# Kernel optimization log

Measured on AMD Instinct MI355X. Metric: run time of the kernel, lower is better.

Reference implementation:

```python
import jax, jax.numpy as jnp
import numpy as np

NUM_CP = 5
DEGREE = 4
GRID_LO, GRID_HI = -1.0, 1.0
G = 3  # grid points, set via set_grid_points(3)


def _precompute_basis():
    # knots = linspace(lo - degree*0.1, hi + degree*0.1, num_cp + degree + 1)
    knots = np.linspace(GRID_LO - DEGREE * 0.1, GRID_HI + DEGREE * 0.1, NUM_CP + DEGREE + 1)
    grid_points = np.linspace(GRID_LO, GRID_HI, G)
    basis = np.zeros((G, NUM_CP), dtype=np.float32)
    for i in range(NUM_CP):
        center = (knots[i + DEGREE // 2] + knots[i + DEGREE // 2 + 1]) / 2.0
        width = (knots[i + DEGREE + 1] - knots[i]) / 2.0
        basis[:, i] = np.exp(-((grid_points - center) / width) ** 2)
    basis_sum = basis.sum(axis=1, keepdims=True)
    return (basis / (basis_sum + 1e-6)).astype(np.float32)


def setup_inputs() -> dict:
    key = jax.random.key(0)
    k1, k2, k3, k4 = jax.random.split(key, 4)
    x = jax.random.normal(k1, (8, 2048, 2048), dtype=jnp.float32)
    control_points = jax.random.normal(k2, (NUM_CP,), dtype=jnp.float32) * 0.1
    base_weight = jax.random.normal(k3, (1,), dtype=jnp.float32)
    spline_weight = jax.random.normal(k4, (1,), dtype=jnp.float32)
    basis_values = jnp.asarray(_precompute_basis())
    return {"x": x, "control_points": control_points, "base_weight": base_weight,
            "spline_weight": spline_weight, "basis_values": basis_values}


def reference(x, control_points, base_weight, spline_weight, basis_values):
    x_clipped = jnp.clip(x, GRID_LO, GRID_HI)
    norm_x = (x_clipped - GRID_LO) / (GRID_HI - GRID_LO)
    grid_idx = norm_x * (G - 1)
    idx_low = jnp.clip(jnp.floor(grid_idx).astype(jnp.int32), 0, G - 1)
    idx_high = jnp.clip(jnp.ceil(grid_idx).astype(jnp.int32), 0, G - 1)
    frac = grid_idx - idx_low.astype(grid_idx.dtype)
    basis_low = basis_values[idx_low]    # [..., NUM_CP]
    basis_high = basis_values[idx_high]  # [..., NUM_CP]
    basis = basis_low * (1.0 - frac[..., None]) + basis_high * frac[..., None]
    y_spline = jnp.einsum('...c,c->...', basis, control_points)
    base = x * jax.nn.sigmoid(x)  # SiLU base_func
    return base_weight * base + spline_weight * y_spline
```

## Files before the change

### kernel.cpp

```cpp
#include <hip/hip_runtime.h>
#include <math.h>


typedef float f32x4 __attribute__((ext_vector_type(4)));

#define TPB 256
#define VPT 4

__device__ __forceinline__ float fast_rcp(float a) {
#if defined(__has_builtin)
#if __has_builtin(__builtin_amdgcn_rcpf)
    return __builtin_amdgcn_rcpf(a);
#else
    return 1.0f / a;
#endif
#else
    return 1.0f / a;
#endif
}

__global__ __launch_bounds__(TPB) void bspline_act_v5(
    const f32x4* __restrict__ x4,
    const float* __restrict__ cp,
    const float* __restrict__ bw_p,
    const float* __restrict__ sw_p,
    const float* __restrict__ bv,
    f32x4*       __restrict__ out4,
    int n4)
{
    const float c0 = cp[0], c1 = cp[1], c2 = cp[2], c3 = cp[3], c4 = cp[4];
    const float s0 = bv[0]*c0  + bv[1]*c1  + bv[2]*c2  + bv[3]*c3  + bv[4]*c4;
    const float s1 = bv[5]*c0  + bv[6]*c1  + bv[7]*c2  + bv[8]*c3  + bv[9]*c4;
    const float s2 = bv[10]*c0 + bv[11]*c1 + bv[12]*c2 + bv[13]*c3 + bv[14]*c4;
    const float bw = bw_p[0], sw = sw_p[0];
    const float S1 = sw * s1;
    const float D0 = sw * (s1 - s0);
    const float D1 = sw * (s2 - s1);

    const int base = blockIdx.x * (TPB * VPT) + threadIdx.x;

    f32x4 v[VPT];
#pragma unroll
    for (int k = 0; k < VPT; ++k) {
        const int idx = base + k * TPB;
        if (idx < n4) {
            v[k] = __builtin_nontemporal_load(&x4[idx]);
        } else {
            f32x4 z = {0.f, 0.f, 0.f, 0.f};
            v[k] = z;
        }
    }

#pragma unroll
    for (int k = 0; k < VPT; ++k) {
        const int idx = base + k * TPB;
        f32x4 xv = v[k];
        f32x4 r;
#pragma unroll
        for (int e = 0; e < 4; ++e) {
            float x  = xv[e];
            float u  = fminf(fmaxf(x, -1.0f), 1.0f);
            float ys = fmaf(D0, fminf(u, 0.0f),
                       fmaf(D1, fmaxf(u, 0.0f), S1));
            float ex  = __expf(-x);
            float sig = fast_rcp(1.0f + ex);
            r[e] = fmaf(bw * x, sig, ys);
        }
        if (idx < n4) __builtin_nontemporal_store(r, &out4[idx]);
    }
}

__global__ void bspline_act_tail(
    const float* __restrict__ x,
    const float* __restrict__ cp,
    const float* __restrict__ bw_p,
    const float* __restrict__ sw_p,
    const float* __restrict__ bv,
    float*       __restrict__ out,
    int start, int n)
{
    int i = start + blockIdx.x * blockDim.x + threadIdx.x;
    if (i >= n) return;
    const float c0 = cp[0], c1 = cp[1], c2 = cp[2], c3 = cp[3], c4 = cp[4];
    const float s0 = bv[0]*c0  + bv[1]*c1  + bv[2]*c2  + bv[3]*c3  + bv[4]*c4;
    const float s1 = bv[5]*c0  + bv[6]*c1  + bv[7]*c2  + bv[8]*c3  + bv[9]*c4;
    const float s2 = bv[10]*c0 + bv[11]*c1 + bv[12]*c2 + bv[13]*c3 + bv[14]*c4;
    const float bw = bw_p[0], sw = sw_p[0];
    const float S1 = sw * s1;
    const float D0 = sw * (s1 - s0);
    const float D1 = sw * (s2 - s1);

    float xv = x[i];
    float u  = fminf(fmaxf(xv, -1.0f), 1.0f);
    float ys = fmaf(D0, fminf(u, 0.0f), fmaf(D1, fmaxf(u, 0.0f), S1));
    float ex  = __expf(-xv);
    float sig = fast_rcp(1.0f + ex);
    out[i] = fmaf(bw * xv, sig, ys);
}

extern "C" void kernel_launch(void* const* d_in, const int* in_sizes, int n_in,
                              void* d_out, int out_size, void* d_ws, size_t ws_size,
                              hipStream_t stream) {
    const float* x  = (const float*)d_in[0];
    const float* cp = (const float*)d_in[1];
    const float* bw = (const float*)d_in[2];
    const float* sw = (const float*)d_in[3];
    const float* bv = (const float*)d_in[4];
    float* out = (float*)d_out;

    const int n  = in_sizes[0];
    const int n4 = n / 4;
    const int rem_start = n4 * 4;

    if (n4 > 0) {
        const int per_block = TPB * VPT;
        const int grid = (n4 + per_block - 1) / per_block;
        bspline_act_v5<<<grid, TPB, 0, stream>>>(
            (const f32x4*)x, cp, bw, sw, bv, (f32x4*)out, n4);
    }
    if (rem_start < n) {
        const int rem = n - rem_start;
        bspline_act_tail<<<(rem + 255) / 256, 256, 0, stream>>>(
            x, cp, bw, sw, bv, out, rem_start, n);
    }
}
```

Before: 226.0 us.

## Switch to grid-stride loop with capped grid and plain loads

Replaces the one-tile-per-block launch with a persistent grid-stride loop capped at a fixed number of blocks, each thread processing four strided vectors per iteration. Loads are now ordinary cached loads instead of nontemporal, and the sigmoid uses a full-precision division instead of the hardware reciprocal builtin. The aim is to cut block launch overhead and keep more loads in flight; the cost is that a fixed grid cap may underfill the device, and the exact division adds extra ALU work.

After: 244.6 us. +8.2%, slower.

```diff
diff --git a/kernel.cpp b/kernel.cpp
--- a/kernel.cpp
+++ b/kernel.cpp
@@ -4,22 +4,11 @@
 
 typedef float f32x4 __attribute__((ext_vector_type(4)));
 
-#define TPB 256
-#define VPT 4
+#define TPB    256
+#define UNROLL 4
+#define MAXBLK 2048
 
-__device__ __forceinline__ float fast_rcp(float a) {
-#if defined(__has_builtin)
-#if __has_builtin(__builtin_amdgcn_rcpf)
-    return __builtin_amdgcn_rcpf(a);
-#else
-    return 1.0f / a;
-#endif
-#else
-    return 1.0f / a;
-#endif
-}
-
-__global__ __launch_bounds__(TPB) void bspline_act_v5(
+__global__ __launch_bounds__(TPB) void bspline_act_v6(
     const f32x4* __restrict__ x4,
     const float* __restrict__ cp,
     const float* __restrict__ bw_p,
@@ -37,24 +26,33 @@
     const float D0 = sw * (s1 - s0);
     const float D1 = sw * (s2 - s1);
 
-    const int base = blockIdx.x * (TPB * VPT) + threadIdx.x;
+    const int stride = gridDim.x * TPB;
+    int i = blockIdx.x * TPB + threadIdx.x;
 
-    f32x4 v[VPT];
+    for (; i + 3 * stride < n4; i += UNROLL * stride) {
+        f32x4 v0 = x4[i];
+        f32x4 v1 = x4[i + stride];
+        f32x4 v2 = x4[i + 2 * stride];
+        f32x4 v3 = x4[i + 3 * stride];
+        f32x4 vin[UNROLL] = {v0, v1, v2, v3};
 #pragma unroll
-    for (int k = 0; k < VPT; ++k) {
-        const int idx = base + k * TPB;
-        if (idx < n4) {
-            v[k] = __builtin_nontemporal_load(&x4[idx]);
-        } else {
-            f32x4 z = {0.f, 0.f, 0.f, 0.f};
-            v[k] = z;
+        for (int k = 0; k < UNROLL; ++k) {
+            f32x4 xv = vin[k];
+            f32x4 r;
+#pragma unroll
+            for (int e = 0; e < 4; ++e) {
+                float x  = xv[e];
+                float u  = fminf(fmaxf(x, -1.0f), 1.0f);
+                float ys = fmaf(D0, fminf(u, 0.0f),
+                           fmaf(D1, fmaxf(u, 0.0f), S1));
+                float sig = 1.0f / (1.0f + __expf(-x));
+                r[e] = fmaf(bw * x, sig, ys);
+            }
+            __builtin_nontemporal_store(r, &out4[i + k * stride]);
         }
     }
-
-#pragma unroll
-    for (int k = 0; k < VPT; ++k) {
-        const int idx = base + k * TPB;
-        f32x4 xv = v[k];
+    for (; i < n4; i += stride) {
+        f32x4 xv = x4[i];
         f32x4 r;
 #pragma unroll
         for (int e = 0; e < 4; ++e) {
@@ -62,11 +60,10 @@
             float u  = fminf(fmaxf(x, -1.0f), 1.0f);
             float ys = fmaf(D0, fminf(u, 0.0f),
                        fmaf(D1, fmaxf(u, 0.0f), S1));
-            float ex  = __expf(-x);
-            float sig = fast_rcp(1.0f + ex);
+            float sig = 1.0f / (1.0f + __expf(-x));
             r[e] = fmaf(bw * x, sig, ys);
         }
-        if (idx < n4) __builtin_nontemporal_store(r, &out4[idx]);
+        __builtin_nontemporal_store(r, &out4[i]);
     }
 }
 
@@ -93,8 +90,7 @@
     float xv = x[i];
     float u  = fminf(fmaxf(xv, -1.0f), 1.0f);
     float ys = fmaf(D0, fminf(u, 0.0f), fmaf(D1, fmaxf(u, 0.0f), S1));
-    float ex  = __expf(-xv);
-    float sig = fast_rcp(1.0f + ex);
+    float sig = 1.0f / (1.0f + __expf(-xv));
     out[i] = fmaf(bw * xv, sig, ys);
 }
 
@@ -113,9 +109,9 @@
     const int rem_start = n4 * 4;
 
     if (n4 > 0) {
-        const int per_block = TPB * VPT;
-        const int grid = (n4 + per_block - 1) / per_block;
-        bspline_act_v5<<<grid, TPB, 0, stream>>>(
+        int grid = (n4 + TPB - 1) / TPB;
+        if (grid > MAXBLK) grid = MAXBLK;
+        bspline_act_v6<<<grid, TPB, 0, stream>>>(
             (const f32x4*)x, cp, bw, sw, bv, (f32x4*)out, n4);
     }
     if (rem_start < n) {
```
